# Optimization experiments

Hardware: AMD Instinct MI355X
Metric: run time of the kernel (lower is better)

Reference implementation:

```python
import jax, jax.numpy as jnp
import numpy as np

D_MODEL = 1024
H = 16
DK = D_MODEL // H


def setup_inputs() -> dict:
    key = jax.random.key(0)
    ks = jax.random.split(key, 13)
    B, S = 2, 2048
    scale = 1.0 / np.sqrt(D_MODEL)
    inp = {
        "query": jax.random.normal(ks[0], (B, S, D_MODEL), jnp.float32),
        "key": jax.random.normal(ks[1], (B, S, D_MODEL), jnp.float32),
        "value": jax.random.normal(ks[2], (B, S, D_MODEL), jnp.float32),
        "mask": jax.random.randint(ks[3], (B, 1, S, S), 0, 2, jnp.int32),
        "Wq": jax.random.normal(ks[4], (D_MODEL, D_MODEL), jnp.float32) * scale,
        "bq": jnp.zeros((D_MODEL,), jnp.float32),
        "Wk": jax.random.normal(ks[5], (D_MODEL, D_MODEL), jnp.float32) * scale,
        "bk": jnp.zeros((D_MODEL,), jnp.float32),
        "Wv": jax.random.normal(ks[6], (D_MODEL, D_MODEL), jnp.float32) * scale,
        "bv": jnp.zeros((D_MODEL,), jnp.float32),
        "Wo": jax.random.normal(ks[7], (D_MODEL, D_MODEL), jnp.float32) * scale,
        "bo": jnp.zeros((D_MODEL,), jnp.float32),
    }
    return inp


def _split_heads(x, W, b):
    # torch Linear: x @ W.T + b; then [B,S,D] -> [B,H,S,DK]
    B, S, _ = x.shape
    out = x @ W.T + b
    return out.reshape(B, S, H, DK).transpose(0, 2, 1, 3)


def reference(query, key, value, mask, Wq, bq, Wk, bk, Wv, bv, Wo, bo):
    B, S, _ = query.shape
    q = _split_heads(query, Wq, bq)   # [B,H,S,DK]
    k = _split_heads(key, Wk, bk)
    v = _split_heads(value, Wv, bv)
    scores = jnp.einsum("bhqd,bhkd->bhqk", q, k) / jnp.sqrt(jnp.asarray(DK, q.dtype))
    scores = jnp.where(mask == 0, jnp.asarray(-1e9, scores.dtype), scores)
    prob = jax.nn.softmax(scores, axis=-1)
    out = jnp.einsum("bhqk,bhkd->bhqd", prob, v)  # [B,H,S,DK]
    out = out.transpose(0, 2, 1, 3).reshape(B, S, D_MODEL)
    return out @ Wo.T + bo
```

## Files before the change

### kernel.cpp

```cpp
#include <hip/hip_runtime.h>
#include <hip/hip_bf16.h>

#define B_   2
#define S_   2048
#define DM   1024
#define NH   16
#define Mdim 4096
#define Kdim 1024

typedef __attribute__((ext_vector_type(8))) short bf16x8;
typedef __attribute__((ext_vector_type(4))) short bf16x4;
typedef __attribute__((ext_vector_type(4))) float f32x4;

__device__ __forceinline__ short f2b(float x) {
  union { __hip_bfloat16 h; short s; } u;
  u.h = __float2bfloat16(x);
  return u.s;
}

__device__ __forceinline__ void async_copy16(const void* g, void* l) {
  __builtin_amdgcn_global_load_lds(
      (const __attribute__((address_space(1))) unsigned int*)g,
      (__attribute__((address_space(3))) unsigned int*)l, 16, 0, 0);
}

struct Cvt7 {
  const float* src[7];
  ushort* dst[7];
  int n[7];
};

__global__ __launch_bounds__(256) void cvt_all(Cvt7 c) {
  const int ten = blockIdx.y;
  const int base = (blockIdx.x * 256 + threadIdx.x) * 8;
  if (base >= c.n[ten]) return;
  const float* s = c.src[ten] + base;
  float4 a = *(const float4*)s;
  float4 b = *(const float4*)(s + 4);
  bf16x8 r;
  r[0] = f2b(a.x); r[1] = f2b(a.y); r[2] = f2b(a.z); r[3] = f2b(a.w);
  r[4] = f2b(b.x); r[5] = f2b(b.y); r[6] = f2b(b.z); r[7] = f2b(b.w);
  *(bf16x8*)(c.dst[ten] + base) = r;
}

__global__ __launch_bounds__(256) void pack_mask(const int* __restrict__ mask,
                                                 unsigned long long* __restrict__ mpk) {
  const int gw = (blockIdx.x * 256 + threadIdx.x) >> 6;
  const int lane = threadIdx.x & 63;
  const int mv = mask[(size_t)gw * 64 + lane];
  const unsigned long long bits = __ballot(mv != 0);
  if (lane == 0) mpk[gw] = bits;
}

template <int MODE>
__global__ __launch_bounds__(256) void gemm_m97(const ushort* __restrict__ A,
                                                const ushort* __restrict__ W,
                                                const float* __restrict__ bias,
                                                void* __restrict__ Cv, float scale) {
  const int t = threadIdx.x;
  const int w = t >> 6, lane = t & 63;
  const int quad = lane >> 4, r16 = lane & 15;
  const int wr = w >> 1, wc = w & 1;
  const int row0 = blockIdx.x * 128, col0 = blockIdx.y * 128;

  __shared__ alignas(16) ushort a_s[128 * 32];
  __shared__ alignas(16) ushort b_s[128 * 32];

  const int sr = t >> 2, sc = (t & 3) * 8;
  const ushort* Ag0 = A + (size_t)(row0 + sr) * Kdim + sc;
  const ushort* Ag1 = Ag0 + (size_t)64 * Kdim;
  const ushort* Wg0 = W + (size_t)(col0 + sr) * Kdim + sc;
  const ushort* Wg1 = Wg0 + (size_t)64 * Kdim;
  ushort* al0 = &a_s[w * 512];
  ushort* al1 = &a_s[2048 + w * 512];
  ushort* bl0 = &b_s[w * 512];
  ushort* bl1 = &b_s[2048 + w * 512];

  f32x4 acc[4][4];
#pragma unroll
  for (int mt = 0; mt < 4; ++mt)
#pragma unroll
    for (int nt = 0; nt < 4; ++nt) acc[mt][nt] = (f32x4){0.f, 0.f, 0.f, 0.f};

  for (int k0 = 0; k0 < Kdim; k0 += 32) {
    __syncthreads();
    async_copy16(Ag0 + k0, al0);
    async_copy16(Ag1 + k0, al1);
    async_copy16(Wg0 + k0, bl0);
    async_copy16(Wg1 + k0, bl1);
    __syncthreads();

    bf16x8 af[4], bfr[4];
#pragma unroll
    for (int mt = 0; mt < 4; ++mt)
      af[mt] = *(const bf16x8*)&a_s[(wr * 64 + mt * 16 + r16) * 32 + quad * 8];
#pragma unroll
    for (int nt = 0; nt < 4; ++nt)
      bfr[nt] = *(const bf16x8*)&b_s[(wc * 64 + nt * 16 + r16) * 32 + quad * 8];
#pragma unroll
    for (int mt = 0; mt < 4; ++mt)
#pragma unroll
      for (int nt = 0; nt < 4; ++nt)
        acc[mt][nt] = __builtin_amdgcn_mfma_f32_16x16x32_bf16(af[mt], bfr[nt],
                                                              acc[mt][nt], 0, 0, 0);
  }

#pragma unroll
  for (int mt = 0; mt < 4; ++mt) {
#pragma unroll
    for (int nt = 0; nt < 4; ++nt) {
      const int col = col0 + wc * 64 + nt * 16 + r16;
      const float bv = bias[col];
      const int rowb = row0 + wr * 64 + mt * 16 + quad * 4;
#pragma unroll
      for (int i = 0; i < 4; ++i) {
        const float v = (acc[mt][nt][i] + bv) * scale;
        const int row = rowb + i;
        if (MODE == 0) {
          ((float*)Cv)[(size_t)row * DM + col] = v;
        } else if (MODE == 1) {
          ((ushort*)Cv)[(size_t)row * DM + col] = (ushort)f2b(v);
        } else if (MODE == 2) {
          const int bb = row >> 11, s = row & (S_ - 1);
          const int hh = col >> 6, d = col & 63;
          const size_t idx = ((size_t)(bb * NH + hh) * S_ + s) * 64 +
                             (((d >> 3) ^ (s & 7)) * 8) + (d & 7);
          ((ushort*)Cv)[idx] = (ushort)f2b(v);
        } else {
          const int bb = row >> 11, s = row & (S_ - 1);
          const int hh = col >> 6, d = col & 63;
          const size_t idx = ((size_t)(bb * NH + hh) * 64 + d) * S_ + (s & ~63) +
                             ((((s >> 3) & 7) ^ (d & 7)) * 8) + (s & 7);
          ((ushort*)Cv)[idx] = (ushort)f2b(v);
        }
      }
    }
  }
}

__global__ __launch_bounds__(256) void attn_mfma(const ushort* __restrict__ Qp,
                                                 const ushort* __restrict__ Kg,
                                                 const ushort* __restrict__ Vg,
                                                 const unsigned long long* __restrict__ mpk,
                                                 ushort* __restrict__ Oa) {
  const int bh = blockIdx.y;
  const int b = bh >> 4, h = bh & 15;
  const int q0 = blockIdx.x * 64;
  const int t = threadIdx.x;
  const int w = t >> 6, lane = t & 63, quad = lane >> 4, r16 = lane & 15;
  const size_t rb = (size_t)b * S_;

  __shared__ alignas(16) ushort k_s[64 * 64];
  __shared__ alignas(16) ushort vt_s[64 * 64];
  __shared__ alignas(16) ushort p_s[4][16 * 76];

  const ushort* qptr = Qp + (rb + q0 + w * 16 + r16) * DM + h * 64 + quad * 8;
  const bf16x8 aq0 = *(const bf16x8*)qptr;
  const bf16x8 aq1 = *(const bf16x8*)(qptr + 32);

  float l_i[4] = {0.f, 0.f, 0.f, 0.f};
  f32x4 oacc[4];
#pragma unroll
  for (int nt = 0; nt < 4; ++nt) oacc[nt] = (f32x4){0.f, 0.f, 0.f, 0.f};

  const int srow = t >> 3, schunk = t & 7;
  const ushort* kgb = Kg + ((size_t)bh * S_ + srow) * 64 + schunk * 8;
  const ushort* vgb = Vg + ((size_t)bh * 64 + srow) * S_ + schunk * 8;
  ushort* kl0 = &k_s[w * 512];
  ushort* kl1 = &k_s[2048 + w * 512];
  ushort* vl0 = &vt_s[w * 512];
  ushort* vl1 = &vt_s[2048 + w * 512];

  const unsigned long long* mrowp = mpk + (rb + q0 + w * 16 + quad * 4) * 32;

  for (int kt = 0; kt < S_; kt += 64) {
    __syncthreads();
    async_copy16(kgb + (size_t)kt * 64, kl0);
    async_copy16(kgb + (size_t)(kt + 32) * 64, kl1);
    async_copy16(vgb + kt, vl0);
    async_copy16(vgb + (size_t)32 * S_ + kt, vl1);
    __syncthreads();

    f32x4 sacc[4];
#pragma unroll
    for (int nt = 0; nt < 4; ++nt) {
      sacc[nt] = (f32x4){0.f, 0.f, 0.f, 0.f};
      const int krow = nt * 16 + r16;
      const bf16x8 b0 = *(const bf16x8*)&k_s[krow * 64 + ((quad ^ (krow & 7)) * 8)];
      const bf16x8 b1 = *(const bf16x8*)&k_s[krow * 64 + (((4 + quad) ^ (krow & 7)) * 8)];
      sacc[nt] = __builtin_amdgcn_mfma_f32_16x16x32_bf16(aq0, b0, sacc[nt], 0, 0, 0);
      sacc[nt] = __builtin_amdgcn_mfma_f32_16x16x32_bf16(aq1, b1, sacc[nt], 0, 0, 0);
    }

    const int seg = kt >> 6;
#pragma unroll
    for (int i = 0; i < 4; ++i) {
      const unsigned long long mbits = mrowp[i * 32 + seg];
      float ps = 0.f;
#pragma unroll
      for (int nt = 0; nt < 4; ++nt) {
        const unsigned int bit = (unsigned int)(mbits >> (nt * 16 + r16)) & 1u;
        const float p = bit ? __expf(sacc[nt][i]) : 0.f;
        ps += p;
        p_s[w][(quad * 4 + i) * 76 + nt * 16 + r16] = (ushort)f2b(p);
      }
      l_i[i] += ps;
    }

#pragma unroll
    for (int ks = 0; ks < 2; ++ks) {
      const bf16x4 lo = *(const bf16x4*)&p_s[w][r16 * 76 + ks * 32 + quad * 8];
      const bf16x4 hi = *(const bf16x4*)&p_s[w][r16 * 76 + ks * 32 + quad * 8 + 4];
      bf16x8 pa;
#pragma unroll
      for (int j = 0; j < 4; ++j) { pa[j] = lo[j]; pa[4 + j] = hi[j]; }
      const int kc = ks * 4 + quad;
#pragma unroll
      for (int nt = 0; nt < 4; ++nt) {
        const int dk = nt * 16 + r16;
        const bf16x8 vb = *(const bf16x8*)&vt_s[dk * 64 + ((kc ^ (dk & 7)) * 8)];
        oacc[nt] = __builtin_amdgcn_mfma_f32_16x16x32_bf16(pa, vb, oacc[nt], 0, 0, 0);
      }
    }
  }

#pragma unroll
  for (int i = 0; i < 4; ++i) {
    float l = l_i[i];
#pragma unroll
    for (int off = 1; off < 16; off <<= 1) l += __shfl_xor(l, off);
    l_i[i] = l;
  }
#pragma unroll
  for (int nt = 0; nt < 4; ++nt) {
#pragma unroll
    for (int i = 0; i < 4; ++i) {
      const int row = q0 + w * 16 + quad * 4 + i;
      const int col = h * 64 + nt * 16 + r16;
      Oa[(rb + row) * DM + col] = (ushort)f2b(oacc[nt][i] / l_i[i]);
    }
  }
}

extern "C" void kernel_launch(void* const* d_in, const int* in_sizes, int n_in,
                              void* d_out, int out_size, void* d_ws, size_t ws_size,
                              hipStream_t stream) {
  const int* mask = (const int*)d_in[3];
  const float* bq = (const float*)d_in[5];
  const float* bk = (const float*)d_in[7];
  const float* bv = (const float*)d_in[9];
  const float* bo = (const float*)d_in[11];

  const size_t NE = (size_t)B_ * S_ * DM;
  const size_t NW = (size_t)DM * DM;

  ushort* qc = (ushort*)d_ws;
  ushort* kc = qc + NE;
  ushort* vc = kc + NE;
  ushort* Qp = vc + NE;
  ushort* Kg = Qp + NE;
  ushort* Vg = Kg + NE;
  ushort* Wqc = Vg + NE;
  ushort* Wkc = Wqc + NW;
  ushort* Wvc = Wkc + NW;
  ushort* Woc = Wvc + NW;
  unsigned long long* mpk = (unsigned long long*)kc;

  Cvt7 c;
  const int sidx[7] = {0, 1, 2, 4, 6, 8, 10};
  ushort* dsts[7] = {qc, kc, vc, Wqc, Wkc, Wvc, Woc};
  for (int i = 0; i < 7; ++i) {
    c.src[i] = (const float*)d_in[sidx[i]];
    c.dst[i] = dsts[i];
    c.n[i] = (i < 3) ? (int)NE : (int)NW;
  }
  cvt_all<<<dim3(2048, 7), 256, 0, stream>>>(c);

  dim3 gg(Mdim / 128, DM / 128);
  gemm_m97<1><<<gg, 256, 0, stream>>>(qc, Wqc, bq, Qp, 0.125f);
  gemm_m97<2><<<gg, 256, 0, stream>>>(kc, Wkc, bk, Kg, 1.0f);
  gemm_m97<3><<<gg, 256, 0, stream>>>(vc, Wvc, bv, Vg, 1.0f);

  pack_mask<<<(B_ * S_ * (S_ / 64) * 64) / 256, 256, 0, stream>>>(mask, mpk);

  attn_mfma<<<dim3(S_ / 64, B_ * NH), 256, 0, stream>>>(Qp, Kg, Vg, mpk, qc);

  gemm_m97<0><<<gg, 256, 0, stream>>>(qc, Woc, bo, (float*)d_out, 1.0f);
}
```

Baseline: 314.4 us.

## Pre-block GEMM operands into tile layout and double-buffer LDS loads

The conversion kernel and the attention output now write bf16 operands in a blocked layout (128-row by 32-k tiles, split into k-quads). Each GEMM tile load is then one contiguous 8 KB chunk, and the LDS fragment reads become conflict-free. The GEMM also double-buffers LDS so the next k-block's async copy is issued before the current block's MFMAs, which drops one barrier per iteration. The cost is a more complex indexing scheme that all producers must follow. The prefetch also relies on the async copies finishing by the next barrier, with no explicit vmcnt wait.

After: 348.6 us. 10.9% more time.

```diff
diff --git a/kernel.cpp b/kernel.cpp
--- a/kernel.cpp
+++ b/kernel.cpp
@@ -16,6 +16,11 @@
   union { __hip_bfloat16 h; short s; } u;
   u.h = __float2bfloat16(x);
   return u.s;
+}
+
+__device__ __forceinline__ size_t blk_idx(int row, int k) {
+  return ((size_t)(row >> 7) * 32 + (k >> 5)) * 4096 + ((k >> 3) & 3) * 1024 +
+         (row & 127) * 8 + (k & 7);
 }
 
 __device__ __forceinline__ void async_copy16(const void* g, void* l) {
@@ -40,7 +45,8 @@
   bf16x8 r;
   r[0] = f2b(a.x); r[1] = f2b(a.y); r[2] = f2b(a.z); r[3] = f2b(a.w);
   r[4] = f2b(b.x); r[5] = f2b(b.y); r[6] = f2b(b.z); r[7] = f2b(b.w);
-  *(bf16x8*)(c.dst[ten] + base) = r;
+  const int row = base >> 10, k = base & 1023;
+  *(bf16x8*)(c.dst[ten] + blk_idx(row, k)) = r;
 }
 
 __global__ __launch_bounds__(256) void pack_mask(const int* __restrict__ mask,
@@ -53,28 +59,31 @@
 }
 
 template <int MODE>
-__global__ __launch_bounds__(256) void gemm_m97(const ushort* __restrict__ A,
-                                                const ushort* __restrict__ W,
-                                                const float* __restrict__ bias,
-                                                void* __restrict__ Cv, float scale) {
+__global__ __launch_bounds__(256) void gemm_pipe(const ushort* __restrict__ A,
+                                                 const ushort* __restrict__ W,
+                                                 const float* __restrict__ bias,
+                                                 void* __restrict__ Cv, float scale) {
   const int t = threadIdx.x;
   const int w = t >> 6, lane = t & 63;
   const int quad = lane >> 4, r16 = lane & 15;
   const int wr = w >> 1, wc = w & 1;
   const int row0 = blockIdx.x * 128, col0 = blockIdx.y * 128;
 
-  __shared__ alignas(16) ushort a_s[128 * 32];
-  __shared__ alignas(16) ushort b_s[128 * 32];
-
-  const int sr = t >> 2, sc = (t & 3) * 8;
-  const ushort* Ag0 = A + (size_t)(row0 + sr) * Kdim + sc;
-  const ushort* Ag1 = Ag0 + (size_t)64 * Kdim;
-  const ushort* Wg0 = W + (size_t)(col0 + sr) * Kdim + sc;
-  const ushort* Wg1 = Wg0 + (size_t)64 * Kdim;
-  ushort* al0 = &a_s[w * 512];
-  ushort* al1 = &a_s[2048 + w * 512];
-  ushort* bl0 = &b_s[w * 512];
-  ushort* bl1 = &b_s[2048 + w * 512];
+  __shared__ alignas(16) ushort a_s[2][4096];
+  __shared__ alignas(16) ushort b_s[2][4096];
+
+  const ushort* Ab = A + (size_t)blockIdx.x * 32 * 4096 + (size_t)t * 8;
+  const ushort* Wb = W + (size_t)blockIdx.y * 32 * 4096 + (size_t)t * 8;
+  const int lo0 = w * 512, lo1 = 2048 + w * 512;
+
+#define STAGE(buf, kb)                                   \
+  do {                                                   \
+    const size_t off = (size_t)(kb) * 4096;              \
+    async_copy16(Ab + off, &a_s[buf][lo0]);              \
+    async_copy16(Ab + off + 2048, &a_s[buf][lo1]);       \
+    async_copy16(Wb + off, &b_s[buf][lo0]);              \
+    async_copy16(Wb + off + 2048, &b_s[buf][lo1]);       \
+  } while (0)
 
   f32x4 acc[4][4];
 #pragma unroll
@@ -82,28 +91,28 @@
 #pragma unroll
     for (int nt = 0; nt < 4; ++nt) acc[mt][nt] = (f32x4){0.f, 0.f, 0.f, 0.f};
 
-  for (int k0 = 0; k0 < Kdim; k0 += 32) {
+  STAGE(0, 0);
+  int cur = 0;
+  for (int kb = 0; kb < 32; ++kb) {
     __syncthreads();
-    async_copy16(Ag0 + k0, al0);
-    async_copy16(Ag1 + k0, al1);
-    async_copy16(Wg0 + k0, bl0);
-    async_copy16(Wg1 + k0, bl1);
-    __syncthreads();
+    if (kb + 1 < 32) STAGE(1 - cur, kb + 1);
 
     bf16x8 af[4], bfr[4];
 #pragma unroll
     for (int mt = 0; mt < 4; ++mt)
-      af[mt] = *(const bf16x8*)&a_s[(wr * 64 + mt * 16 + r16) * 32 + quad * 8];
+      af[mt] = *(const bf16x8*)&a_s[cur][quad * 1024 + (wr * 64 + mt * 16 + r16) * 8];
 #pragma unroll
     for (int nt = 0; nt < 4; ++nt)
-      bfr[nt] = *(const bf16x8*)&b_s[(wc * 64 + nt * 16 + r16) * 32 + quad * 8];
+      bfr[nt] = *(const bf16x8*)&b_s[cur][quad * 1024 + (wc * 64 + nt * 16 + r16) * 8];
 #pragma unroll
     for (int mt = 0; mt < 4; ++mt)
 #pragma unroll
       for (int nt = 0; nt < 4; ++nt)
         acc[mt][nt] = __builtin_amdgcn_mfma_f32_16x16x32_bf16(af[mt], bfr[nt],
                                                               acc[mt][nt], 0, 0, 0);
-  }
+    cur ^= 1;
+  }
+#undef STAGE
 
 #pragma unroll
   for (int mt = 0; mt < 4; ++mt) {
@@ -163,9 +172,8 @@
 #pragma unroll
   for (int nt = 0; nt < 4; ++nt) oacc[nt] = (f32x4){0.f, 0.f, 0.f, 0.f};
 
-  const int srow = t >> 3, schunk = t & 7;
-  const ushort* kgb = Kg + ((size_t)bh * S_ + srow) * 64 + schunk * 8;
-  const ushort* vgb = Vg + ((size_t)bh * 64 + srow) * S_ + schunk * 8;
+  const ushort* kgb = Kg + (size_t)bh * S_ * 64 + (size_t)t * 8;
+  const ushort* vgb = Vg + (size_t)bh * 64 * S_ + (size_t)(t >> 3) * S_ + (t & 7) * 8;
   ushort* kl0 = &k_s[w * 512];
   ushort* kl1 = &k_s[2048 + w * 512];
   ushort* vl0 = &vt_s[w * 512];
@@ -235,9 +243,9 @@
   for (int nt = 0; nt < 4; ++nt) {
 #pragma unroll
     for (int i = 0; i < 4; ++i) {
-      const int row = q0 + w * 16 + quad * 4 + i;
+      const int row = (int)rb + q0 + w * 16 + quad * 4 + i;
       const int col = h * 64 + nt * 16 + r16;
-      Oa[(rb + row) * DM + col] = (ushort)f2b(oacc[nt][i] / l_i[i]);
+      Oa[blk_idx(row, col)] = (ushort)f2b(oacc[nt][i] / l_i[i]);
     }
   }
 }
@@ -277,13 +285,13 @@
   cvt_all<<<dim3(2048, 7), 256, 0, stream>>>(c);
 
   dim3 gg(Mdim / 128, DM / 128);
-  gemm_m97<1><<<gg, 256, 0, stream>>>(qc, Wqc, bq, Qp, 0.125f);
-  gemm_m97<2><<<gg, 256, 0, stream>>>(kc, Wkc, bk, Kg, 1.0f);
-  gemm_m97<3><<<gg, 256, 0, stream>>>(vc, Wvc, bv, Vg, 1.0f);
+  gemm_pipe<1><<<gg, 256, 0, stream>>>(qc, Wqc, bq, Qp, 0.125f);
+  gemm_pipe<2><<<gg, 256, 0, stream>>>(kc, Wkc, bk, Kg, 1.0f);
+  gemm_pipe<3><<<gg, 256, 0, stream>>>(vc, Wvc, bv, Vg, 1.0f);
 
   pack_mask<<<(B_ * S_ * (S_ / 64) * 64) / 256, 256, 0, stream>>>(mask, mpk);
 
   attn_mfma<<<dim3(S_ / 64, B_ * NH), 256, 0, stream>>>(Qp, Kg, Vg, mpk, qc);
 
-  gemm_m97<0><<<gg, 256, 0, stream>>>(qc, Woc, bo, (float*)d_out, 1.0f);
-}
+  gemm_pipe<0><<<gg, 256, 0, stream>>>(qc, Woc, bo, (float*)d_out, 1.0f);
+}
```
